# Optimization experiments

Hardware: AMD Instinct MI355X
Metric: run time of the kernel (lower is better)

## Reference

```python
import jax, jax.numpy as jnp
import numpy as np

HEADS = 20  # SDXL-style: hidden_size 1280 / head_dim 64
IP_SCALE = 1.0


def setup_inputs() -> dict:
    key = jax.random.key(0)
    ks = jax.random.split(key, 12)
    B, Sq, T, C, D, NIP = 4, 4096, 77, 1280, 2048, 16
    s = lambda fan: 1.0 / np.sqrt(fan)
    # post-softmax multiplicative mask: col 0 (sot token) forced to 1, rest a binary spatial mask
    spat = (jax.random.uniform(ks[0], (1, Sq, 1)) < 0.5).astype(jnp.float32)
    attention_mask = jnp.concatenate([jnp.ones((1, Sq, 1)), jnp.tile(spat, (1, 1, T - 1))], axis=-1)
    return {
        "hidden_states": jax.random.normal(ks[1], (B, Sq, C), jnp.float32),
        "encoder_hidden_states": jax.random.normal(ks[2], (B, T, D), jnp.float32),
        "ip_hidden_states": jax.random.normal(ks[3], (B, NIP, D), jnp.float32),
        "attention_mask": attention_mask,
        "Wq": jax.random.normal(ks[4], (C, C), jnp.float32) * s(C),
        "Wk": jax.random.normal(ks[5], (D, C), jnp.float32) * s(D),
        "Wv": jax.random.normal(ks[6], (D, C), jnp.float32) * s(D),
        "Wo": jax.random.normal(ks[7], (C, C), jnp.float32) * s(C),
        "bo": jnp.zeros((C,), jnp.float32),
        "Wk_ip": jax.random.normal(ks[8], (D, C), jnp.float32) * s(D),
        "Wv_ip": jax.random.normal(ks[9], (D, C), jnp.float32) * s(D),
    }


def reference(hidden_states, encoder_hidden_states, ip_hidden_states, attention_mask,
              Wq, Wk, Wv, Wo, bo, Wk_ip, Wv_ip):
    B, Sq, C = hidden_states.shape
    H = HEADS
    d = C // H
    scale = d ** -0.5
    # projections (torch Linear with weights stored [in, out])
    q = (hidden_states @ Wq).reshape(B, Sq, H, d)
    k = (encoder_hidden_states @ Wk).reshape(B, -1, H, d)
    v = (encoder_hidden_states @ Wv).reshape(B, -1, H, d)
    # explicit QK^T softmax, then POST-softmax multiplicative mask (as in get_attention_scores + mask multiply)
    scores = jnp.einsum('bqhd,bkhd->bhqk', q, k) * scale
    probs = jax.nn.softmax(scores, axis=-1)
    probs = probs * attention_mask[:, None, :, :]  # [1,1,Sq,T] broadcast over batch*heads
    out = jnp.einsum('bhqk,bkhd->bqhd', probs, v).reshape(B, Sq, C)
    out = out @ Wo + bo  # to_out[0]; to_out[1] is dropout (identity at eval)
    # IP-adapter stream (single stream, no spatial ip mask): standard SDPA against ip tokens
    k_ip = (ip_hidden_states @ Wk_ip).reshape(B, -1, H, d)
    v_ip = (ip_hidden_states @ Wv_ip).reshape(B, -1, H, d)
    s_ip = jnp.einsum('bqhd,bkhd->bhqk', q, k_ip) * scale
    p_ip = jax.nn.softmax(s_ip, axis=-1)
    ip_out = jnp.einsum('bhqk,bkhd->bqhd', p_ip, v_ip).reshape(B, Sq, C)
    return out + IP_SCALE * ip_out
```

## Files before the change

kernel.cpp:

```cpp
#include <hip/hip_runtime.h>

typedef __attribute__((ext_vector_type(4))) float f32x4;
typedef __attribute__((ext_vector_type(8))) short s16x8;
typedef __attribute__((ext_vector_type(8))) __bf16 bf16x8;
typedef unsigned short u16;

__device__ __forceinline__ u16 f2b(float f) {
  union { float f; unsigned u; } x; x.f = f;
  unsigned r = x.u + 0x7fffu + ((x.u >> 16) & 1u);
  return (u16)(r >> 16);
}
__device__ __forceinline__ float b2f(u16 u) {
  union { unsigned u; float f; } x; x.u = ((unsigned)u) << 16;
  return x.f;
}
__device__ __forceinline__ void gld16(const void* g, void* l) {
  __builtin_amdgcn_global_load_lds(
      (const __attribute__((address_space(1))) unsigned int*)g,
      (__attribute__((address_space(3))) unsigned int*)l, 16, 0, 0);
}
__device__ __forceinline__ f32x4 mfma_bf16(s16x8 a, s16x8 b, f32x4 c) {
  return __builtin_amdgcn_mfma_f32_16x16x32_bf16(
      __builtin_bit_cast(bf16x8, a), __builtin_bit_cast(bf16x8, b), c, 0, 0, 0);
}

#define BAR() asm volatile("s_barrier" ::: "memory")

__global__ void k_convert_all(const float* __restrict__ hs, const float* __restrict__ ehs,
                              const float* __restrict__ iph,
                              u16* __restrict__ hsb, u16* __restrict__ ehsb,
                              u16* __restrict__ ipb) {
  const int n1 = 16384 * 1280 / 4, n2 = 308 * 2048 / 4, n3 = 64 * 2048 / 4;
  int i = blockIdx.x * blockDim.x + threadIdx.x;
  const float* src; u16* dst; int j = i;
  if (i < n1) { src = hs; dst = hsb; }
  else if (i < n1 + n2) { src = ehs; dst = ehsb; j = i - n1; }
  else if (i < n1 + n2 + n3) { src = iph; dst = ipb; j = i - n1 - n2; }
  else return;
  float4 v = ((const float4*)src)[j];
  ushort4 o;
  o.x = f2b(v.x); o.y = f2b(v.y); o.z = f2b(v.z); o.w = f2b(v.w);
  ((ushort4*)dst)[j] = o;
}

__device__ __forceinline__ void transpose_tile(const float* __restrict__ W,
                                               u16* __restrict__ WT, int K, int N) {
  __shared__ float tile[32][33];
  int n0 = blockIdx.x * 32, k0 = blockIdx.y * 32;
  int tx = threadIdx.x & 31, ty = threadIdx.x >> 5;
#pragma unroll
  for (int i = 0; i < 32; i += 8)
    tile[ty + i][tx] = W[(size_t)(k0 + ty + i) * N + n0 + tx];
  __syncthreads();
#pragma unroll
  for (int i = 0; i < 32; i += 8)
    WT[(size_t)(n0 + ty + i) * K + k0 + tx] = f2b(tile[tx][ty + i]);
}

__global__ void k_transpose4(const float* W0, const float* W1, const float* W2,
                             const float* W3, u16* T0, u16* T1, u16* T2, u16* T3,
                             int K, int N) {
  int z = blockIdx.z;
  const float* W = (z == 0) ? W0 : (z == 1) ? W1 : (z == 2) ? W2 : W3;
  u16* T = (z == 0) ? T0 : (z == 1) ? T1 : (z == 2) ? T2 : T3;
  transpose_tile(W, T, K, N);
}
__global__ void k_transpose2(const float* W0, const float* W1, u16* T0, u16* T1,
                             int K, int N) {
  int z = blockIdx.z;
  transpose_tile(z ? W1 : W0, z ? T1 : T0, K, N);
}

__device__ __forceinline__ void gemm_core0(
    const u16* __restrict__ A, const u16* __restrict__ BT,
    int M, int N, int K, u16* __restrict__ outb, int m0, int n0) {
  const int tid = threadIdx.x;
  const int l = tid & 63;
  const int w = tid >> 6;
  const int wr = w >> 1, wc = w & 1;
  __shared__ u16 As[128 * 32];
  __shared__ u16 Bs[128 * 32];
  f32x4 acc[4][4] = {};

  const int o0 = tid * 16;
  const int o1 = o0 + 4096;
  const int ra0 = o0 >> 6, ca0 = (o0 & 63) >> 1;
  const int ra1 = o1 >> 6, ca1 = (o1 & 63) >> 1;
  int ga0 = m0 + ra0; if (ga0 >= M) ga0 = M - 1;
  int ga1 = m0 + ra1; if (ga1 >= M) ga1 = M - 1;
  const u16* Ar0 = A + (size_t)ga0 * K + ca0;
  const u16* Ar1 = A + (size_t)ga1 * K + ca1;
  const u16* Br0 = BT + (size_t)(n0 + ra0) * K + ca0;
  const u16* Br1 = BT + (size_t)(n0 + ra1) * K + ca1;

  for (int k0 = 0; k0 < K; k0 += 32) {
    gld16(Ar0 + k0, &As[o0 >> 1]);
    gld16(Ar1 + k0, &As[o1 >> 1]);
    gld16(Br0 + k0, &Bs[o0 >> 1]);
    gld16(Br1 + k0, &Bs[o1 >> 1]);
    __syncthreads();
    s16x8 af[4], bfr[4];
#pragma unroll
    for (int mi = 0; mi < 4; ++mi)
      af[mi] = *(const s16x8*)&As[(wr * 64 + mi * 16 + (l & 15)) * 32 + (l >> 4) * 8];
#pragma unroll
    for (int ni = 0; ni < 4; ++ni)
      bfr[ni] = *(const s16x8*)&Bs[(wc * 64 + ni * 16 + (l & 15)) * 32 + (l >> 4) * 8];
#pragma unroll
    for (int mi = 0; mi < 4; ++mi)
#pragma unroll
      for (int ni = 0; ni < 4; ++ni)
        acc[mi][ni] = mfma_bf16(af[mi], bfr[ni], acc[mi][ni]);
    __syncthreads();
  }

#pragma unroll
  for (int mi = 0; mi < 4; ++mi) {
    const int mbase = m0 + wr * 64 + mi * 16 + (l >> 4) * 4;
#pragma unroll
    for (int ni = 0; ni < 4; ++ni) {
      const int ncol = n0 + wc * 64 + ni * 16 + (l & 15);
#pragma unroll
      for (int r = 0; r < 4; ++r) {
        int m = mbase + r;
        if (m < M) outb[(size_t)m * N + ncol] = f2b(acc[mi][ni][r]);
      }
    }
  }
}

__global__ __launch_bounds__(256) void k_gemm_small4(
    const u16* __restrict__ ehsb, const u16* __restrict__ ipb,
    const u16* __restrict__ WkT, const u16* __restrict__ WvT,
    const u16* __restrict__ WkipT, const u16* __restrict__ WvipT,
    u16* kbuf, u16* vbuf, u16* kipb, u16* vipb) {
  const int z = blockIdx.z;
  const int M = (z < 2) ? 308 : 64;
  const int m0 = blockIdx.y * 128;
  if (m0 >= M) return;
  const u16* A = (z < 2) ? ehsb : ipb;
  const u16* BT = (z == 0) ? WkT : (z == 1) ? WvT : (z == 2) ? WkipT : WvipT;
  u16* out = (z == 0) ? kbuf : (z == 1) ? vbuf : (z == 2) ? kipb : vipb;
  gemm_core0(A, BT, M, 1280, 2048, out, m0, blockIdx.x * 128);
}

template <int EPI>
__global__ __launch_bounds__(512, 1) void k_gemm256(
    const u16* __restrict__ A, const u16* __restrict__ BT,
    int N, int K, float alpha,
    u16* __restrict__ outb, float* __restrict__ outf,
    const float* __restrict__ bias, const u16* __restrict__ ipadd,
    int nbx) {
  __shared__ u16 lds[73728];
  const int tid = threadIdx.x, l = tid & 63, w = tid >> 6;
  const int lr = l & 15, lg = l >> 4;
  const int wr = w >> 2, wc = w & 3;
  const bool wlo = (w < 4);

  const int nwg = gridDim.x;
  const int q = nwg >> 3, r = nwg & 7;
  const int xcd = blockIdx.x & 7, lid = blockIdx.x >> 3;
  const int wg = (xcd < r) ? (xcd * (q + 1) + lid)
                           : (r * (q + 1) + (xcd - r) * q + lid);
  const int bm0 = (wg / nbx) * 256, bn0 = (wg % nbx) * 320;

  const int srow = tid >> 2;
  const int sslot = ((tid & 3) ^ ((srow >> 1) & 3)) * 8;
  const size_t aO0 = (size_t)(bm0 + srow) * K + sslot;
  const size_t aO1 = aO0 + (size_t)128 * K;
  const size_t bO0 = (size_t)(bn0 + srow) * K + sslot;
  const size_t bO1 = bO0 + (size_t)128 * K;
  const size_t bO2 = bO0 + (size_t)256 * K;
  const int d0 = tid * 8, d1 = (tid + 512) * 8, d2 = (tid + 1024) * 8;

  const int KT = K >> 5;
  f32x4 acc[8][5] = {};
  s16x8 bfv[5], afv[4];

  const int xsw = (lg ^ ((lr >> 1) & 3)) * 8;
  const int aRow = (wr * 128 + lr) * 32 + xsw;
  const int bRow = 32768 + (wc * 80 + lr) * 32 + xsw;

#define STAGE_A(slot, kt)                                              \
  {                                                                    \
    const int base_ = (slot) * 8192;                                   \
    const size_t go_ = (size_t)(kt) * 32;                              \
    gld16(A + aO0 + go_, &lds[base_ + d0]);                            \
    gld16(A + aO1 + go_, &lds[base_ + d1]);                            \
  }
#define STAGE_B(slot, kt)                                              \
  {                                                                    \
    const int base_ = 32768 + (slot) * 10240;                          \
    const size_t go_ = (size_t)(kt) * 32;                              \
    gld16(BT + bO0 + go_, &lds[base_ + d0]);                           \
    gld16(BT + bO1 + go_, &lds[base_ + d1]);                           \
    if (wlo) gld16(BT + bO2 + go_, &lds[base_ + d2]);                  \
  }
#define WAIT_DEEP()                                                    \
  {                                                                    \
    if (wlo) asm volatile("s_waitcnt vmcnt(10)" ::: "memory");         \
    else     asm volatile("s_waitcnt vmcnt(8)" ::: "memory");          \
  }
#define WAIT_MID()                                                     \
  {                                                                    \
    if (wlo) asm volatile("s_waitcnt vmcnt(5)" ::: "memory");          \
    else     asm volatile("s_waitcnt vmcnt(4)" ::: "memory");          \
  }
#define WAITVM0() asm volatile("s_waitcnt vmcnt(0)" ::: "memory")

  STAGE_A(0, 0); STAGE_B(0, 0);
  STAGE_A(1, 1); STAGE_B(1, 1);
  STAGE_A(2, 2); STAGE_B(2, 2);
  WAIT_DEEP();
  BAR();

  for (int j = 0; j < KT; ++j) {
    const int slot = j & 3;
    const int ab = slot * 8192;
    const int bb = slot * 10240;
    const bool pf = (j + 3 < KT);
    const int s3 = (j + 3) & 3;
#pragma unroll
    for (int ni = 0; ni < 5; ++ni)
      bfv[ni] = *(const s16x8*)&lds[bb + bRow + ni * 512];
#pragma unroll
    for (int mi = 0; mi < 4; ++mi)
      afv[mi] = *(const s16x8*)&lds[ab + aRow + mi * 512];
    if (pf) STAGE_A(s3, j + 3);
    __builtin_amdgcn_s_setprio(1);
#pragma unroll
    for (int mi = 0; mi < 4; ++mi)
#pragma unroll
      for (int ni = 0; ni < 5; ++ni)
        acc[mi][ni] = mfma_bf16(afv[mi], bfv[ni], acc[mi][ni]);
    __builtin_amdgcn_s_setprio(0);
#pragma unroll
    for (int mi = 0; mi < 4; ++mi)
      afv[mi] = *(const s16x8*)&lds[ab + aRow + (mi + 4) * 512];
    if (pf) STAGE_B(s3, j + 3);
    __builtin_amdgcn_s_setprio(1);
#pragma unroll
    for (int mi = 0; mi < 4; ++mi)
#pragma unroll
      for (int ni = 0; ni < 5; ++ni)
        acc[mi + 4][ni] = mfma_bf16(afv[mi], bfv[ni], acc[mi + 4][ni]);
    __builtin_amdgcn_s_setprio(0);
    if (pf) { WAIT_DEEP(); }
    else if (j == KT - 3) { WAIT_MID(); }
    else { WAITVM0(); }
    BAR();
  }

  WAITVM0();
  __syncthreads();

  if constexpr (EPI == 0) {
#pragma unroll
    for (int half = 0; half < 2; ++half) {
      if (half) __syncthreads();
      if (wr == half) {
#pragma unroll
        for (int mi = 0; mi < 8; ++mi) {
          const int row = mi * 16 + lg * 4;
#pragma unroll
          for (int ni = 0; ni < 5; ++ni) {
            const int col = wc * 80 + ni * 16 + lr;
#pragma unroll
            for (int rr = 0; rr < 4; ++rr)
              lds[(row + rr) * 320 + col] = f2b(acc[mi][ni][rr] * alpha);
          }
        }
      }
      __syncthreads();
      const int rbase = tid >> 3;
      const int cseg = tid & 7;
#pragma unroll
      for (int rr2 = 0; rr2 < 2; ++rr2)
#pragma unroll
        for (int jj = 0; jj < 5; ++jj) {
          const int row = rr2 * 64 + rbase;
          const int ch = cseg + jj * 8;
          *(int4*)(outb + (size_t)(bm0 + half * 128 + row) * N + bn0 + ch * 8) =
              *(const int4*)&lds[row * 320 + ch * 8];
        }
    }
  } else {
#pragma unroll
    for (int mi = 0; mi < 8; ++mi) {
      const int mrow = bm0 + wr * 128 + mi * 16 + lg * 4;
#pragma unroll
      for (int ni = 0; ni < 5; ++ni) {
        const int ncol = bn0 + wc * 80 + ni * 16 + lr;
#pragma unroll
        for (int rr = 0; rr < 4; ++rr) {
          const size_t idx = (size_t)(mrow + rr) * N + ncol;
          outf[idx] = acc[mi][ni][rr] + bias[ncol] + b2f(ipadd[idx]);
        }
      }
    }
  }
#undef STAGE_A
#undef STAGE_B
#undef WAIT_DEEP
#undef WAIT_MID
#undef WAITVM0
}

__global__ __launch_bounds__(512, 4) void k_attn(
    const u16* __restrict__ Q,
    const u16* __restrict__ Kb,
    const u16* __restrict__ Vb,
    const u16* __restrict__ Kip,
    const u16* __restrict__ Vip,
    const float* __restrict__ mask,
    u16* __restrict__ Oattn,
    u16* __restrict__ Oip) {
  const int qt = blockIdx.x, h = blockIdx.y, b = blockIdx.z;
  const int tid = threadIdx.x, l = tid & 63, w = tid >> 6;
  const int lr = l & 15, lg = l >> 4;
  const int r0 = w * 16;
  const int m0 = b * 4096 + qt * 128;

  __shared__ u16 KV[192][72];
  __shared__ u16 Ps[128][104];
  __shared__ u16 P2s[128][40];

  const u16* qrow = Q + (size_t)(m0 + r0 + lr) * 1280 + h * 64;
  s16x8 aq0 = *(const s16x8*)(qrow + lg * 8);
  s16x8 aq1 = *(const s16x8*)(qrow + 32 + lg * 8);

  for (int s = tid; s < 192 * 8; s += 512) {
    const int row = s >> 3, seg = s & 7;
    int4 v = {0, 0, 0, 0};
    const u16* src = nullptr;
    if (row < 77)       src = Kb  + (size_t)(b * 77 + row) * 1280 + h * 64 + seg * 8;
    else if (row < 80)  src = nullptr;
    else if (row < 96)  src = Kip + (size_t)(b * 16 + row - 80) * 1280 + h * 64 + seg * 8;
    else if (row < 173) src = Vb  + (size_t)(b * 77 + row - 96) * 1280 + h * 64 + seg * 8;
    else if (row < 176) src = nullptr;
    else                src = Vip + (size_t)(b * 16 + row - 176) * 1280 + h * 64 + seg * 8;
    if (src) v = *(const int4*)src;
    *(int4*)&KV[row][(seg ^ ((row >> 3) & 3)) * 8] = v;
  }
  __syncthreads();

  f32x4 sc[5];
  f32x4 sip = {};
#pragma unroll
  for (int t5 = 0; t5 < 6; ++t5) {
    const int trow = t5 * 16 + lr;
    const int qz = (trow >> 3) & 3;
    s16x8 b0 = *(const s16x8*)&KV[trow][(lg ^ qz) * 8];
    s16x8 b1 = *(const s16x8*)&KV[trow][((lg + 4) ^ qz) * 8];
    f32x4 c = {};
    c = mfma_bf16(aq0, b0, c);
    c = mfma_bf16(aq1, b1, c);
    if (t5 < 5) sc[t5] = c; else sip = c;
  }

#pragma unroll
  for (int r = 0; r < 4; ++r) {
    float mx = fmaxf(fmaxf(fmaxf(sc[0][r], sc[1][r]), fmaxf(sc[2][r], sc[3][r])), sc[4][r]);
    mx = fmaxf(mx, __shfl_xor(mx, 1));
    mx = fmaxf(mx, __shfl_xor(mx, 2));
    mx = fmaxf(mx, __shfl_xor(mx, 4));
    mx = fmaxf(mx, __shfl_xor(mx, 8));
    float p[5], sm = 0.f;
#pragma unroll
    for (int t5 = 0; t5 < 5; ++t5) {
      bool valid = (t5 < 4) | (lr < 13);
      p[t5] = valid ? __expf(sc[t5][r] - mx) : 0.f;
      sm += p[t5];
    }
    sm += __shfl_xor(sm, 1);
    sm += __shfl_xor(sm, 2);
    sm += __shfl_xor(sm, 4);
    sm += __shfl_xor(sm, 8);
    const float inv = 1.0f / sm;
    const int row = r0 + lg * 4 + r;
    const int qg = qt * 128 + row;
#pragma unroll
    for (int t5 = 0; t5 < 5; ++t5) {
      int t = t5 * 16 + lr;
      float pf = 0.f;
      if (t < 77) pf = p[t5] * inv * mask[qg * 77 + t];
      Ps[row][t] = f2b(pf);
    }
    Ps[row][80 + lr] = 0;

    float m2 = sip[r];
    m2 = fmaxf(m2, __shfl_xor(m2, 1));
    m2 = fmaxf(m2, __shfl_xor(m2, 2));
    m2 = fmaxf(m2, __shfl_xor(m2, 4));
    m2 = fmaxf(m2, __shfl_xor(m2, 8));
    float pi = __expf(sip[r] - m2);
    float s2 = pi;
    s2 += __shfl_xor(s2, 1);
    s2 += __shfl_xor(s2, 2);
    s2 += __shfl_xor(s2, 4);
    s2 += __shfl_xor(s2, 8);
    P2s[row][lr] = 0;
    P2s[row][16 + lr] = f2b(pi / s2);
  }

  s16x8 ap[3];
#pragma unroll
  for (int ks = 0; ks < 3; ++ks)
    ap[ks] = *(const s16x8*)&Ps[r0 + lr][ks * 32 + lg * 8];
  s16x8 aip = *(const s16x8*)&P2s[r0 + lr][lg * 8];

  f32x4 om[4], oi[4];
#pragma unroll
  for (int nt = 0; nt < 4; ++nt) {
    const int dcol = (nt * 16 + lr) ^ (lg << 3);
    f32x4 o = {};
#pragma unroll
    for (int ks = 0; ks < 3; ++ks) {
      s16x8 bv;
#pragma unroll
      for (int j = 0; j < 8; ++j)
        bv[j] = (short)KV[96 + ks * 32 + lg * 8 + j][dcol];
      o = mfma_bf16(ap[ks], bv, o);
    }
    s16x8 bip;
#pragma unroll
    for (int j = 0; j < 8; ++j)
      bip[j] = (short)KV[160 + lg * 8 + j][dcol];
    f32x4 o2 = {};
    o2 = mfma_bf16(aip, bip, o2);
    om[nt] = o;
    oi[nt] = o2;
  }

  __syncthreads();

  u16 (*Om)[72] = (u16(*)[72]) & KV[0][0];
  u16 (*Oi)[72] = (u16(*)[72]) & Ps[0][0];
#pragma unroll
  for (int nt = 0; nt < 4; ++nt)
#pragma unroll
    for (int r = 0; r < 4; ++r) {
      const int row = r0 + lg * 4 + r;
      const int d = nt * 16 + lr;
      Om[row][d] = f2b(om[nt][r]);
      Oi[row][d] = f2b(oi[nt][r]);
    }
  __syncthreads();

  for (int s = tid; s < 128 * 8; s += 512) {
    const int row = s >> 3, seg = s & 7;
    const size_t g = (size_t)(m0 + row) * 1280 + h * 64 + seg * 8;
    *(int4*)(Oattn + g) = *(const int4*)&Om[row][seg * 8];
    *(int4*)(Oip + g) = *(const int4*)&Oi[row][seg * 8];
  }
}

extern "C" void kernel_launch(void* const* d_in, const int* in_sizes, int n_in,
                              void* d_out, int out_size, void* d_ws, size_t ws_size,
                              hipStream_t stream) {
  (void)in_sizes; (void)n_in; (void)out_size; (void)ws_size;
  const float* hs   = (const float*)d_in[0];
  const float* ehs  = (const float*)d_in[1];
  const float* iph  = (const float*)d_in[2];
  const float* mask = (const float*)d_in[3];
  const float* Wq   = (const float*)d_in[4];
  const float* Wk   = (const float*)d_in[5];
  const float* Wv   = (const float*)d_in[6];
  const float* Wo   = (const float*)d_in[7];
  const float* bo   = (const float*)d_in[8];
  const float* Wkip = (const float*)d_in[9];
  const float* Wvip = (const float*)d_in[10];
  float* out = (float*)d_out;

  char* ws = (char*)d_ws;
  size_t off = 0;
  auto alloc = [&](size_t bytes) {
    char* p = ws + off;
    off += (bytes + 255) & ~(size_t)255;
    return p;
  };
  u16* hsb   = (u16*)alloc(16384ull * 1280 * 2);
  u16* qbuf  = (u16*)alloc(16384ull * 1280 * 2);
  u16* ipout = (u16*)alloc(16384ull * 1280 * 2);
  u16* WqT   = (u16*)alloc(1280ull * 1280 * 2);
  u16* WoT   = (u16*)alloc(1280ull * 1280 * 2);
  u16* WkT   = (u16*)alloc(1280ull * 2048 * 2);
  u16* WvT   = (u16*)alloc(1280ull * 2048 * 2);
  u16* WkipT = (u16*)alloc(1280ull * 2048 * 2);
  u16* WvipT = (u16*)alloc(1280ull * 2048 * 2);
  u16* ehsb  = (u16*)alloc(308ull * 2048 * 2);
  u16* ipb   = (u16*)alloc(64ull * 2048 * 2);
  u16* kbuf  = (u16*)alloc(308ull * 1280 * 2);
  u16* vbuf  = (u16*)alloc(308ull * 1280 * 2);
  u16* kipb  = (u16*)alloc(64ull * 1280 * 2);
  u16* vipb  = (u16*)alloc(64ull * 1280 * 2);

  const int ntot4 = (16384 * 1280 + 308 * 2048 + 64 * 2048) / 4;
  k_convert_all<<<(ntot4 + 255) / 256, 256, 0, stream>>>(hs, ehs, iph, hsb, ehsb, ipb);
  k_transpose4<<<dim3(40, 64, 4), 256, 0, stream>>>(Wk, Wv, Wkip, Wvip,
                                                    WkT, WvT, WkipT, WvipT, 2048, 1280);
  k_transpose2<<<dim3(40, 40, 2), 256, 0, stream>>>(Wq, Wo, WqT, WoT, 1280, 1280);

  k_gemm256<0><<<256, 512, 0, stream>>>(hsb, WqT, 1280, 1280, 0.125f,
                                        qbuf, nullptr, nullptr, nullptr, 4);
  k_gemm_small4<<<dim3(10, 3, 4), 256, 0, stream>>>(ehsb, ipb, WkT, WvT, WkipT, WvipT,
                                                    kbuf, vbuf, kipb, vipb);

  k_attn<<<dim3(32, 20, 4), 512, 0, stream>>>(qbuf, kbuf, vbuf, kipb, vipb, mask,
                                              hsb, ipout);

  k_gemm256<1><<<256, 512, 0, stream>>>(hsb, WoT, 1280, 1280, 1.f,
                                        nullptr, out, bo, ipout, 4);
}
```

Measured before the change: 265.4 us.

## Double-buffer GEMM LDS fragments in registers and unroll the K loop by four

Rewrites the bf16 GEMM main loop so the A and B fragments for the next K tile are read from LDS into a second register set while the current tile's MFMAs run. The loop is unrolled by four with sched_barriers to pin the order of LDS reads, global-to-LDS prefetch and MFMA groups. Both A and B prefetches are now issued together at the start of each step. The vmcnt wait is relaxed so that one prefetch stage stays in flight instead of two. This aims to hide LDS read latency behind the matrix cores, but it raises register pressure and assumes KT is a multiple of four.

```diff
diff --git a/kernel.cpp b/kernel.cpp
--- a/kernel.cpp
+++ b/kernel.cpp
@@ -175,12 +175,13 @@
 
   const int KT = K >> 5;
   f32x4 acc[8][5] = {};
-  s16x8 bfv[5], afv[4];
+  s16x8 aLo[4], aHi[4], Bc0[5], Bc1[5];
 
   const int xsw = (lg ^ ((lr >> 1) & 3)) * 8;
-  const int aRow = (wr * 128 + lr) * 32 + xsw;
-  const int bRow = 32768 + (wc * 80 + lr) * 32 + xsw;
-
+  const int aR = (wr * 128 + lr) * 32 + xsw;
+  const int bR = (wc * 80 + lr) * 32 + xsw;
+
+#define SB0() __builtin_amdgcn_sched_barrier(0)
 #define STAGE_A(slot, kt)                                              \
   {                                                                    \
     const int base_ = (slot) * 8192;                                   \
@@ -196,62 +197,73 @@
     gld16(BT + bO1 + go_, &lds[base_ + d1]);                           \
     if (wlo) gld16(BT + bO2 + go_, &lds[base_ + d2]);                  \
   }
-#define WAIT_DEEP()                                                    \
-  {                                                                    \
-    if (wlo) asm volatile("s_waitcnt vmcnt(10)" ::: "memory");         \
-    else     asm volatile("s_waitcnt vmcnt(8)" ::: "memory");          \
-  }
-#define WAIT_MID()                                                     \
+#define WAIT1()                                                        \
   {                                                                    \
     if (wlo) asm volatile("s_waitcnt vmcnt(5)" ::: "memory");          \
     else     asm volatile("s_waitcnt vmcnt(4)" ::: "memory");          \
   }
-#define WAITVM0() asm volatile("s_waitcnt vmcnt(0)" ::: "memory")
+#define VM0() asm volatile("s_waitcnt vmcnt(0)" ::: "memory")
 
   STAGE_A(0, 0); STAGE_B(0, 0);
   STAGE_A(1, 1); STAGE_B(1, 1);
   STAGE_A(2, 2); STAGE_B(2, 2);
-  WAIT_DEEP();
+  WAIT1();
   BAR();
-
-  for (int j = 0; j < KT; ++j) {
-    const int slot = j & 3;
-    const int ab = slot * 8192;
-    const int bb = slot * 10240;
-    const bool pf = (j + 3 < KT);
-    const int s3 = (j + 3) & 3;
-#pragma unroll
-    for (int ni = 0; ni < 5; ++ni)
-      bfv[ni] = *(const s16x8*)&lds[bb + bRow + ni * 512];
-#pragma unroll
-    for (int mi = 0; mi < 4; ++mi)
-      afv[mi] = *(const s16x8*)&lds[ab + aRow + mi * 512];
-    if (pf) STAGE_A(s3, j + 3);
-    __builtin_amdgcn_s_setprio(1);
-#pragma unroll
-    for (int mi = 0; mi < 4; ++mi)
-#pragma unroll
-      for (int ni = 0; ni < 5; ++ni)
-        acc[mi][ni] = mfma_bf16(afv[mi], bfv[ni], acc[mi][ni]);
-    __builtin_amdgcn_s_setprio(0);
-#pragma unroll
-    for (int mi = 0; mi < 4; ++mi)
-      afv[mi] = *(const s16x8*)&lds[ab + aRow + (mi + 4) * 512];
-    if (pf) STAGE_B(s3, j + 3);
-    __builtin_amdgcn_s_setprio(1);
-#pragma unroll
-    for (int mi = 0; mi < 4; ++mi)
-#pragma unroll
-      for (int ni = 0; ni < 5; ++ni)
-        acc[mi + 4][ni] = mfma_bf16(afv[mi], bfv[ni], acc[mi + 4][ni]);
-    __builtin_amdgcn_s_setprio(0);
-    if (pf) { WAIT_DEEP(); }
-    else if (j == KT - 3) { WAIT_MID(); }
-    else { WAITVM0(); }
-    BAR();
-  }
-
-  WAITVM0();
+#pragma unroll
+  for (int m = 0; m < 4; ++m)
+    aLo[m] = *(const s16x8*)&lds[aR + m * 512];
+#pragma unroll
+  for (int n = 0; n < 5; ++n)
+    Bc0[n] = *(const s16x8*)&lds[32768 + bR + n * 512];
+
+#define TILE_BODY(u, Bcur, Bnxt)                                        \
+  {                                                                     \
+    const int j = it * 4 + (u);                                         \
+    const int sa = (u) * 8192;                                          \
+    const int nu = ((u) + 1) & 3;                                       \
+    const int na = nu * 8192;                                           \
+    const int nb = 32768 + nu * 10240;                                  \
+    const bool pf = (j + 3 < KT);                                       \
+    SB0();                                                              \
+    _Pragma("unroll")                                                   \
+    for (int m = 0; m < 4; ++m)                                         \
+      aHi[m] = *(const s16x8*)&lds[sa + aR + (m + 4) * 512];            \
+    SB0();                                                              \
+    if (pf) { STAGE_A(((u) + 3) & 3, j + 3); STAGE_B(((u) + 3) & 3, j + 3); } \
+    SB0();                                                              \
+    __builtin_amdgcn_s_setprio(1);                                      \
+    _Pragma("unroll")                                                   \
+    for (int m = 0; m < 4; ++m)                                         \
+      _Pragma("unroll")                                                 \
+      for (int n = 0; n < 5; ++n)                                       \
+        acc[m][n] = mfma_bf16(aLo[m], Bcur[n], acc[m][n]);              \
+    __builtin_amdgcn_s_setprio(0);                                      \
+    SB0();                                                              \
+    _Pragma("unroll")                                                   \
+    for (int m = 0; m < 4; ++m)                                         \
+      aLo[m] = *(const s16x8*)&lds[na + aR + m * 512];                  \
+    _Pragma("unroll")                                                   \
+    for (int n = 0; n < 5; ++n)                                         \
+      Bnxt[n] = *(const s16x8*)&lds[nb + bR + n * 512];                 \
+    SB0();                                                              \
+    __builtin_amdgcn_s_setprio(1);                                      \
+    _Pragma("unroll")                                                   \
+    for (int m = 0; m < 4; ++m)                                         \
+      _Pragma("unroll")                                                 \
+      for (int n = 0; n < 5; ++n)                                       \
+        acc[m + 4][n] = mfma_bf16(aHi[m], Bcur[n], acc[m + 4][n]);      \
+    __builtin_amdgcn_s_setprio(0);                                      \
+    if (pf) { WAIT1(); } else { VM0(); }                                \
+    BAR();                                                              \
+  }
+
+  for (int it = 0; it < KT / 4; ++it) {
+    TILE_BODY(0, Bc0, Bc1);
+    TILE_BODY(1, Bc1, Bc0);
+    TILE_BODY(2, Bc0, Bc1);
+    TILE_BODY(3, Bc1, Bc0);
+  }
+
   __syncthreads();
 
   if constexpr (EPI == 0) {
@@ -299,11 +311,12 @@
       }
     }
   }
+#undef SB0
 #undef STAGE_A
 #undef STAGE_B
-#undef WAIT_DEEP
-#undef WAIT_MID
-#undef WAITVM0
+#undef WAIT1
+#undef VM0
+#undef TILE_BODY
 }
 
 __global__ __launch_bounds__(512, 4) void k_attn(
```

Result: slower. 573.7 us (+116.2%).
